# Performance work log

Measured on AMD Instinct MI355X. Metric: run time of the kernel, lower is better.

The kernel has to match this reference:

```python
import jax, jax.numpy as jnp
import numpy as np

B, H, W, C, HEADS, WS, SS = 32, 56, 56, 512, 16, 7, 3
HID = 4 * C
N = WS * WS          # tokens per window = 49
NW = (H // WS) * (W // WS)  # windows per image = 64
HD = C // HEADS
SCALE = HD ** -0.5

def _rel_index():
    coords = np.stack(np.meshgrid(np.arange(WS), np.arange(WS), indexing='ij'))
    cf = coords.reshape(2, -1)
    rel = (cf[:, :, None] - cf[:, None, :]).transpose(1, 2, 0)
    rel[..., 0] += WS - 1
    rel[..., 1] += WS - 1
    rel[..., 0] *= 2 * WS - 1
    return rel.sum(-1)  # [N, N]

REL_IDX = _rel_index()

def _attn_mask():
    # standard Swin SW-MSA mask: label 3x3 shifted regions, diff labels -> -100
    img = np.zeros((H, W), dtype=np.float32)
    cnt = 0
    for hs in (slice(0, -WS), slice(-WS, -SS), slice(-SS, None)):
        for ws_ in (slice(0, -WS), slice(-WS, -SS), slice(-SS, None)):
            img[hs, ws_] = cnt
            cnt += 1
    mw = img.reshape(H // WS, WS, W // WS, WS).transpose(0, 2, 1, 3).reshape(NW, N)
    diff = mw[:, None, :] - mw[:, :, None]
    return jnp.asarray(np.where(diff != 0, -100.0, 0.0).astype(np.float32))  # [NW, N, N]

ATTN_MASK = _attn_mask()

def layernorm(x, g, b, eps=1e-5):
    m = jnp.mean(x, -1, keepdims=True)
    v = jnp.mean((x - m) ** 2, -1, keepdims=True)
    return (x - m) * jax.lax.rsqrt(v + eps) * g + b

def setup_inputs():
    key = jax.random.key(0)
    ks = jax.random.split(key, 8)
    f32 = jnp.float32
    return {
        'x': jax.random.normal(ks[0], (B, H * W, C), f32),
        'norm1_g': jnp.ones((C,), f32), 'norm1_b': jnp.zeros((C,), f32),
        'qkv_w': jax.random.normal(ks[1], (3 * C, C), f32) * 0.02,
        'qkv_b': jnp.zeros((3 * C,), f32),
        'rel_bias': jax.random.normal(ks[2], ((2 * WS - 1) ** 2, HEADS), f32) * 0.02,
        'proj_w': jax.random.normal(ks[3], (C, C), f32) * 0.02,
        'proj_b': jnp.zeros((C,), f32),
        'norm2_g': jnp.ones((C,), f32), 'norm2_b': jnp.zeros((C,), f32),
        'mlp_w1': jax.random.normal(ks[4], (HID, C), f32) * 0.02,
        'mlp_b1': jnp.zeros((HID,), f32),
        'mlp_w2': jax.random.normal(ks[5], (C, HID), f32) * 0.02,
        'mlp_b2': jnp.zeros((C,), f32),
    }

def reference(x, norm1_g, norm1_b, qkv_w, qkv_b, rel_bias, proj_w, proj_b,
              norm2_g, norm2_b, mlp_w1, mlp_b1, mlp_w2, mlp_b2):
    skip = x
    h = layernorm(x, norm1_g, norm1_b).reshape(B, H, W, C)
    h = jnp.roll(h, (-SS, -SS), axis=(1, 2))  # cyclic shift
    # window partition -> [B*NW, N, C]
    h = h.reshape(B, H // WS, WS, W // WS, WS, C).transpose(0, 1, 3, 2, 4, 5).reshape(B * NW, N, C)
    qkv = (h @ qkv_w.T + qkv_b).reshape(B * NW, N, 3, HEADS, HD).transpose(2, 0, 3, 1, 4)
    q, k, v = qkv[0] * SCALE, qkv[1], qkv[2]  # [B*NW, HEADS, N, HD]
    attn = jnp.einsum('whnd,whmd->whnm', q, k)
    bias = rel_bias[REL_IDX.reshape(-1)].reshape(N, N, HEADS).transpose(2, 0, 1)
    attn = attn + bias[None]
    attn = attn.reshape(B, NW, HEADS, N, N) + ATTN_MASK[None, :, None]
    attn = jax.nn.softmax(attn, axis=-1).reshape(B * NW, HEADS, N, N)
    h = jnp.einsum('whnm,whmd->whnd', attn, v).transpose(0, 2, 1, 3).reshape(B * NW, N, C)
    h = h @ proj_w.T + proj_b
    # window reverse + reverse cyclic shift
    h = h.reshape(B, H // WS, W // WS, WS, WS, C).transpose(0, 1, 3, 2, 4, 5).reshape(B, H, W, C)
    h = jnp.roll(h, (SS, SS), axis=(1, 2)).reshape(B, H * W, C)
    x = skip + h
    m = layernorm(x, norm2_g, norm2_b)
    m = jax.nn.gelu(m @ mlp_w1.T + mlp_b1, approximate=False) @ mlp_w2.T + mlp_b2
    return x + m
```

## Files before the change

kernel.cpp:

```cpp
#include <hip/hip_runtime.h>
#include <cstdint>
#include <cstddef>

#define DI __device__ __forceinline__

typedef __bf16 bf16_t;
typedef __bf16 bf16x8 __attribute__((ext_vector_type(8)));
typedef float f32x4 __attribute__((ext_vector_type(4)));

static constexpr float SCALE = 0.17677669529663687f;

DI bf16_t f2b(float f) {
  uint32_t u = __builtin_bit_cast(uint32_t, f);
  u += 0x7fffu + ((u >> 16) & 1u);
  return __builtin_bit_cast(bf16_t, (uint16_t)(u >> 16));
}

DI void gld16(const void* g, void* l) {
  __builtin_amdgcn_global_load_lds(
      (const __attribute__((address_space(1))) uint32_t*)g,
      (__attribute__((address_space(3))) uint32_t*)l, 16, 0, 0);
}

__global__ __launch_bounds__(256)
void cvtw(const float* __restrict__ in, bf16_t* __restrict__ out, int n) {
  int i = (blockIdx.x * 256 + threadIdx.x) * 4;
  if (i >= n) return;
  float4 v = *(const float4*)(in + i);
  ushort4 o;
  o.x = __builtin_bit_cast(uint16_t, f2b(v.x));
  o.y = __builtin_bit_cast(uint16_t, f2b(v.y));
  o.z = __builtin_bit_cast(uint16_t, f2b(v.z));
  o.w = __builtin_bit_cast(uint16_t, f2b(v.w));
  *(ushort4*)(out + i) = o;
}

__global__ __launch_bounds__(256)
void bias_pre(const float* __restrict__ rel, float* __restrict__ bf) {
  int idx = blockIdx.x * 256 + threadIdx.x;
  int head = idx >> 12, t1 = (idx >> 6) & 63, t2 = idx & 63;
  float v = -1e30f;
  if (t1 < 49 && t2 < 49) {
    int i1 = t1 / 7, j1 = t1 - i1 * 7, i2 = t2 / 7, j2 = t2 - i2 * 7;
    v = rel[((i1 - i2 + 6) * 13 + (j1 - j2 + 6)) * 16 + head];
  }
  bf[idx] = v;
}

template<bool WIN>
__global__ __launch_bounds__(128)
void ln_kernel(const float* __restrict__ in, const float* __restrict__ g,
               const float* __restrict__ be, bf16_t* __restrict__ out)
{
  const int r = blockIdx.x;
  const int tid = threadIdx.x;
  long srow;
  if (WIN) {
    int bw = r / 49, t = r - bw * 49;
    int b = bw >> 6, w = bw & 63;
    int wh = w >> 3, ww = w & 7;
    int i = t / 7, j = t - i * 7;
    int hs = wh * 7 + i + 3; if (hs >= 56) hs -= 56;
    int wsr = ww * 7 + j + 3; if (wsr >= 56) wsr -= 56;
    srow = (long)b * 3136 + hs * 56 + wsr;
  } else {
    srow = r;
  }
  const float4 v = *(const float4*)(in + srow * 512 + tid * 4);
  float s = v.x + v.y + v.z + v.w;
  float sq = v.x * v.x + v.y * v.y + v.z * v.z + v.w * v.w;
#pragma unroll
  for (int m = 1; m < 64; m <<= 1) { s += __shfl_xor(s, m); sq += __shfl_xor(sq, m); }
  __shared__ float ls[2], lq[2];
  if ((tid & 63) == 0) { ls[tid >> 6] = s; lq[tid >> 6] = sq; }
  __syncthreads();
  s = ls[0] + ls[1]; sq = lq[0] + lq[1];
  const float mean = s * (1.f / 512.f);
  const float rs = rsqrtf(sq * (1.f / 512.f) - mean * mean + 1e-5f);
  const float4 gg = *(const float4*)(g + tid * 4);
  const float4 bb = *(const float4*)(be + tid * 4);
  ushort4 o;
  o.x = __builtin_bit_cast(uint16_t, f2b((v.x - mean) * rs * gg.x + bb.x));
  o.y = __builtin_bit_cast(uint16_t, f2b((v.y - mean) * rs * gg.y + bb.y));
  o.z = __builtin_bit_cast(uint16_t, f2b((v.z - mean) * rs * gg.z + bb.z));
  o.w = __builtin_bit_cast(uint16_t, f2b((v.w - mean) * rs * gg.w + bb.w));
  *(ushort4*)(out + (long)r * 512 + tid * 4) = o;
}

template<int EPI>
__global__ __launch_bounds__(512, 4)
void gemm128(const bf16_t* __restrict__ A, const bf16_t* __restrict__ Bw,
             const float* __restrict__ bias, const float* __restrict__ extra,
             void* __restrict__ out0, void* __restrict__ out1v, void* __restrict__ out2v,
             const int K, const int NBN)
{
  __shared__ __align__(128) bf16_t lds[3][384 * 32];
  const int tid = threadIdx.x, lane = tid & 63, wave = tid >> 6;

  const int nwg = gridDim.x;
  const int q = nwg >> 3, r = nwg & 7;
  const int xcd = blockIdx.x & 7, sidx = blockIdx.x >> 3;
  const int wgid = (xcd < r ? xcd * (q + 1) : r * (q + 1) + (xcd - r) * q) + sidx;
  const int bm = wgid / NBN, bn = wgid - bm * NBN;

  const int scc = ((tid & 3) ^ ((tid >> 3) & 3)) * 8;
  const bf16_t* pA  = A  + (size_t)(bm * 128 + (tid >> 2)) * K + scc;
  const bf16_t* pB0 = Bw + (size_t)(bn * 256 + (tid >> 2)) * K + scc;
  const bf16_t* pB1 = Bw + (size_t)(bn * 256 + 128 + (tid >> 2)) * K + scc;
  const int NT = K >> 5;

#define STAGE(KT, S) do { \
    gld16(pA  + (size_t)(KT) * 32, &lds[S][tid * 8]); \
    gld16(pB0 + (size_t)(KT) * 32, &lds[S][(512 + tid) * 8]); \
    gld16(pB1 + (size_t)(KT) * 32, &lds[S][(1024 + tid) * 8]); \
  } while (0)

  const int fr = lane & 15, fkc = lane >> 4;
  const int swzoff = ((fkc ^ ((fr >> 1) & 3)) << 3);
  const int wr = wave >> 2, wc = wave & 3;

  f32x4 acc[4][4] = {};

  STAGE(0, 0);
  STAGE(1, 1);
  asm volatile("s_waitcnt vmcnt(3)");
  __builtin_amdgcn_s_barrier();
  __builtin_amdgcn_sched_barrier(0);

  for (int t = 0; t < NT; ++t) {
    const int cur = t % 3;
    if (t + 2 < NT) {
      int sb = cur + 2; if (sb >= 3) sb -= 3;
      STAGE(t + 2, sb);
    }
    bf16x8 af[4], bf[4];
#pragma unroll
    for (int m = 0; m < 4; ++m)
      af[m] = *(const bf16x8*)&lds[cur][(wr * 64 + m * 16 + fr) * 32 + swzoff];
#pragma unroll
    for (int n = 0; n < 4; ++n)
      bf[n] = *(const bf16x8*)&lds[cur][(128 + wc * 64 + n * 16 + fr) * 32 + swzoff];
    asm volatile("s_waitcnt lgkmcnt(0)");
    __builtin_amdgcn_sched_barrier(0);
    __builtin_amdgcn_s_setprio(1);
#pragma unroll
    for (int m = 0; m < 4; ++m)
#pragma unroll
      for (int n = 0; n < 4; ++n)
        acc[m][n] = __builtin_amdgcn_mfma_f32_16x16x32_bf16(af[m], bf[n], acc[m][n], 0, 0, 0);
    __builtin_amdgcn_s_setprio(0);
    __builtin_amdgcn_sched_barrier(0);
    if (t + 2 < NT)      asm volatile("s_waitcnt vmcnt(3)");
    else if (t + 1 < NT) asm volatile("s_waitcnt vmcnt(0)");
    __builtin_amdgcn_s_barrier();
    __builtin_amdgcn_sched_barrier(0);
  }
#undef STAGE

  const int rq = fkc * 4;
#pragma unroll
  for (int m = 0; m < 4; ++m) {
#pragma unroll
    for (int j = 0; j < 4; ++j) {
      const int grow = bm * 128 + wr * 64 + m * 16 + rq + j;
      long obase = 0;
      if (EPI == 0) {
        int bwi = grow / 49, t = grow - bwi * 49;
        obase = ((long)bwi * 16 * 49 + t) * 32;
      } else if (EPI == 1) {
        int bwi = grow / 49, t = grow - bwi * 49;
        int b = bwi >> 6, w = bwi & 63;
        int wh = w >> 3, ww = w & 7;
        int i = t / 7, jj = t - i * 7;
        int hs = wh * 7 + i + 3; if (hs >= 56) hs -= 56;
        int wsr = ww * 7 + jj + 3; if (wsr >= 56) wsr -= 56;
        obase = ((long)b * 3136 + hs * 56 + wsr) * 512;
      } else if (EPI == 2) {
        obase = (long)grow * 2048;
      } else {
        obase = (long)grow * 512;
      }
#pragma unroll
      for (int n = 0; n < 4; ++n) {
        const int gcol = bn * 256 + wc * 64 + n * 16 + fr;
        float v = acc[m][n][j] + bias[gcol];
        if (EPI == 0) {
          int part = gcol >> 9, head = (gcol >> 5) & 15, d = gcol & 31;
          if (part == 0) v *= SCALE;
          bf16_t* dst = (bf16_t*)(part == 0 ? out0 : (part == 1 ? out1v : out2v));
          dst[obase + (long)head * (49 * 32) + d] = f2b(v);
        } else if (EPI == 1) {
          ((float*)out0)[obase + gcol] = v + extra[obase + gcol];
        } else if (EPI == 2) {
          float z = 1.5957691216057308f * (v + 0.044715f * v * v * v);
          float e = __expf(z);
          float th = 1.f - 2.f / (e + 1.f);
          float gv = 0.5f * v * (1.f + th);
          ((bf16_t*)out0)[obase + gcol] = f2b(gv);
        } else {
          ((float*)out0)[obase + gcol] = v + extra[obase + gcol];
        }
      }
    }
  }
}

__global__ __launch_bounds__(256)
void attn_kernel(const bf16_t* __restrict__ qb, const bf16_t* __restrict__ kb,
                 const bf16_t* __restrict__ vb, const float* __restrict__ biasf,
                 bf16_t* __restrict__ aout)
{
  __shared__ bf16_t Q[64 * 32];
  __shared__ bf16_t Kl[64 * 32];
  __shared__ bf16_t Vt[32 * 64];
  __shared__ bf16_t Pl[4][16 * 64];
  const int bid = blockIdx.x;
  const int bw = bid >> 4, head = bid & 15;
  const int tid = threadIdx.x, lane = tid & 63, wave = tid >> 6;
  {
    uint4 z = {0u, 0u, 0u, 0u};
    *(uint4*)&Q[tid * 8] = z;
    *(uint4*)&Kl[tid * 8] = z;
    *(uint4*)&Vt[tid * 8] = z;
  }
  __syncthreads();
  const bf16_t* qsrc = qb + (long)bid * (49 * 32);
  const bf16_t* ksrc = kb + (long)bid * (49 * 32);
  const bf16_t* vsrc = vb + (long)bid * (49 * 32);
  if (tid < 196) {
    *(uint4*)&Q[tid * 8] = *(const uint4*)(qsrc + tid * 8);
    *(uint4*)&Kl[tid * 8] = *(const uint4*)(ksrc + tid * 8);
  }
  for (int e = tid; e < 1568; e += 256) {
    int t = e >> 5, d = e & 31;
    Vt[d * 64 + t] = vsrc[e];
  }
  __syncthreads();
  const int fr = lane & 15, fk = (lane >> 4) * 8, rq = (lane >> 4) * 4;
  bf16x8 aq = *(const bf16x8*)&Q[(wave * 16 + fr) * 32 + fk];
  f32x4 s[4];
#pragma unroll
  for (int n = 0; n < 4; ++n) {
    bf16x8 bk = *(const bf16x8*)&Kl[(n * 16 + fr) * 32 + fk];
    f32x4 z = {0.f, 0.f, 0.f, 0.f};
    s[n] = __builtin_amdgcn_mfma_f32_16x16x32_bf16(aq, bk, z, 0, 0, 0);
  }
  const int w = bw & 63;
  const bool wh7 = ((w >> 3) == 7), ww7 = ((w & 7) == 7);
  const float* bh = biasf + head * 4096;
#pragma unroll
  for (int j = 0; j < 4; ++j) {
    const int row = wave * 16 + rq + j;
    int i1 = row / 7, j1 = row - i1 * 7;
    bool b1h = wh7 && (i1 >= 4), b1w = ww7 && (j1 >= 4);
    float pv[4];
    float mx = -3.0e38f;
#pragma unroll
    for (int n = 0; n < 4; ++n) {
      const int col = n * 16 + fr;
      float v = s[n][j] + bh[row * 64 + col];
      if (wh7 || ww7) {
        int i2 = col / 7, j2 = col - i2 * 7;
        bool b2h = wh7 && (i2 >= 4), b2w = ww7 && (j2 >= 4);
        if ((b1h != b2h) || (b1w != b2w)) v -= 100.f;
      }
      pv[n] = v;
      mx = fmaxf(mx, v);
    }
#pragma unroll
    for (int msk = 1; msk < 16; msk <<= 1) mx = fmaxf(mx, __shfl_xor(mx, msk));
    float sm = 0.f;
#pragma unroll
    for (int n = 0; n < 4; ++n) { pv[n] = __expf(pv[n] - mx); sm += pv[n]; }
#pragma unroll
    for (int msk = 1; msk < 16; msk <<= 1) sm += __shfl_xor(sm, msk);
    const float inv = 1.f / sm;
#pragma unroll
    for (int n = 0; n < 4; ++n)
      Pl[wave][(rq + j) * 64 + n * 16 + fr] = f2b(pv[n] * inv);
  }
  __syncthreads();
  f32x4 o[2] = {};
#pragma unroll
  for (int kk = 0; kk < 2; ++kk) {
    bf16x8 pa = *(const bf16x8*)&Pl[wave][fr * 64 + kk * 32 + fk];
#pragma unroll
    for (int dt = 0; dt < 2; ++dt) {
      bf16x8 vv = *(const bf16x8*)&Vt[(dt * 16 + fr) * 64 + kk * 32 + fk];
      o[dt] = __builtin_amdgcn_mfma_f32_16x16x32_bf16(pa, vv, o[dt], 0, 0, 0);
    }
  }
#pragma unroll
  for (int j = 0; j < 4; ++j) {
    const int t1 = wave * 16 + rq + j;
    if (t1 < 49) {
      bf16_t* dst = aout + ((long)bw * 49 + t1) * 512 + head * 32;
      dst[fr] = f2b(o[0][j]);
      dst[16 + fr] = f2b(o[1][j]);
    }
  }
}

extern "C" void kernel_launch(void* const* d_in, const int* in_sizes, int n_in,
                              void* d_out, int out_size, void* d_ws, size_t ws_size,
                              hipStream_t stream)
{
  const float* x      = (const float*)d_in[0];
  const float* n1g    = (const float*)d_in[1];
  const float* n1b    = (const float*)d_in[2];
  const float* qkv_w  = (const float*)d_in[3];
  const float* qkv_b  = (const float*)d_in[4];
  const float* rel    = (const float*)d_in[5];
  const float* proj_w = (const float*)d_in[6];
  const float* proj_b = (const float*)d_in[7];
  const float* n2g    = (const float*)d_in[8];
  const float* n2b    = (const float*)d_in[9];
  const float* w1     = (const float*)d_in[10];
  const float* b1     = (const float*)d_in[11];
  const float* w2     = (const float*)d_in[12];
  const float* b2     = (const float*)d_in[13];

  char* ws = (char*)d_ws;
  bf16_t* Wqkv  = (bf16_t*)(ws + 0);
  bf16_t* Wproj = (bf16_t*)(ws + 1572864);
  bf16_t* Wm1   = (bf16_t*)(ws + 2097152);
  bf16_t* Wm2   = (bf16_t*)(ws + 4194304);
  float*  biasf = (float*)(ws + 6291456);
  const size_t ABYTES = (size_t)100352 * 512 * 2;
  const size_t P1 = 8388608;
  const size_t P2 = P1 + ABYTES + 1048576;
  bf16_t* xw      = (bf16_t*)(ws + P1);
  bf16_t* qbuf    = (bf16_t*)(ws + P2);
  bf16_t* kbuf    = (bf16_t*)(ws + P2 + ABYTES);
  bf16_t* vbuf    = (bf16_t*)(ws + P2 + 2 * ABYTES);
  bf16_t* attnout = xw;
  bf16_t* h2      = xw;
  bf16_t* hidden  = qbuf;

  cvtw<<<768, 256, 0, stream>>>(qkv_w, Wqkv, 1536 * 512);
  cvtw<<<256, 256, 0, stream>>>(proj_w, Wproj, 512 * 512);
  cvtw<<<1024, 256, 0, stream>>>(w1, Wm1, 2048 * 512);
  cvtw<<<1024, 256, 0, stream>>>(w2, Wm2, 512 * 2048);
  bias_pre<<<256, 256, 0, stream>>>(rel, biasf);

  ln_kernel<true><<<100352, 128, 0, stream>>>(x, n1g, n1b, xw);
  gemm128<0><<<784 * 6, 512, 0, stream>>>(xw, Wqkv, qkv_b, nullptr,
                                          qbuf, kbuf, vbuf, 512, 6);
  attn_kernel<<<32768, 256, 0, stream>>>(qbuf, kbuf, vbuf, biasf, attnout);
  gemm128<1><<<784 * 2, 512, 0, stream>>>(attnout, Wproj, proj_b, x,
                                          d_out, nullptr, nullptr, 512, 2);
  ln_kernel<false><<<100352, 128, 0, stream>>>((const float*)d_out, n2g, n2b, h2);
  gemm128<2><<<784 * 8, 512, 0, stream>>>(h2, Wm1, b1, nullptr,
                                          hidden, nullptr, nullptr, 512, 8);
  gemm128<3><<<784 * 2, 512, 0, stream>>>(hidden, Wm2, b2, (const float*)d_out,
                                          d_out, nullptr, nullptr, 2048, 2);
}
```

Before: 1.347 ms.

## Enlarge GEMM tiles to 256x256 with phased double-buffered K=64 pipeline

Replaces the 128x256 GEMM with a 256x256 tile per workgroup. It uses a K=64 step split into two 32-wide halves, double-buffered in LDS, with loads interleaved between four MFMA phases. Each wave now holds 8x4 accumulators, which doubles operand reuse per LDS read and halves the workgroup count. Occupancy drops to 2 waves per SIMD and register pressure goes up. The GELU epilogue is also simplified to use a fast reciprocal, and the bias loads are hoisted out of the row loop.

```diff
diff --git a/kernel.cpp b/kernel.cpp
--- a/kernel.cpp
+++ b/kernel.cpp
@@ -87,14 +87,16 @@
   *(ushort4*)(out + (long)r * 512 + tid * 4) = o;
 }
 
+#define MFMA16(a, b, c) __builtin_amdgcn_mfma_f32_16x16x32_bf16((a), (b), (c), 0, 0, 0)
+
 template<int EPI>
-__global__ __launch_bounds__(512, 4)
-void gemm128(const bf16_t* __restrict__ A, const bf16_t* __restrict__ Bw,
+__global__ __launch_bounds__(512, 2)
+void gemm256(const bf16_t* __restrict__ A, const bf16_t* __restrict__ Bw,
              const float* __restrict__ bias, const float* __restrict__ extra,
              void* __restrict__ out0, void* __restrict__ out1v, void* __restrict__ out2v,
              const int K, const int NBN)
 {
-  __shared__ __align__(128) bf16_t lds[3][384 * 32];
+  __shared__ __align__(128) bf16_t lds[8][8192];
   const int tid = threadIdx.x, lane = tid & 63, wave = tid >> 6;
 
   const int nwg = gridDim.x;
@@ -103,70 +105,121 @@
   const int wgid = (xcd < r ? xcd * (q + 1) : r * (q + 1) + (xcd - r) * q) + sidx;
   const int bm = wgid / NBN, bn = wgid - bm * NBN;
 
-  const int scc = ((tid & 3) ^ ((tid >> 3) & 3)) * 8;
-  const bf16_t* pA  = A  + (size_t)(bm * 128 + (tid >> 2)) * K + scc;
-  const bf16_t* pB0 = Bw + (size_t)(bn * 256 + (tid >> 2)) * K + scc;
-  const bf16_t* pB1 = Bw + (size_t)(bn * 256 + 128 + (tid >> 2)) * K + scc;
-  const int NT = K >> 5;
-
-#define STAGE(KT, S) do { \
-    gld16(pA  + (size_t)(KT) * 32, &lds[S][tid * 8]); \
-    gld16(pB0 + (size_t)(KT) * 32, &lds[S][(512 + tid) * 8]); \
-    gld16(pB1 + (size_t)(KT) * 32, &lds[S][(1024 + tid) * 8]); \
+  const int srow = tid >> 2, slot = tid & 3;
+  const int chunk = slot ^ ((srow >> 1) & 3);
+  const bf16_t* pA = A + (size_t)(bm * 256 + srow) * K + chunk * 8;
+  const bf16_t* pB = Bw + (size_t)(bn * 256 + srow) * K + chunk * 8;
+  const size_t rowK = (size_t)128 * K;
+  const int NT = K >> 6;
+
+#define STG(mat, b, h, koff) do { \
+    const bf16_t* _p = ((mat) ? pB : pA) + (koff); \
+    bf16_t* _l = &lds[((mat) ? 4 : 0) + (b) * 2 + (h)][tid * 8]; \
+    gld16(_p, _l); \
+    gld16(_p + rowK, _l + 4096); \
   } while (0)
 
+  STG(0, 0, 0, 0);  STG(1, 0, 0, 0);
+  STG(0, 0, 1, 32); STG(1, 0, 1, 32);
+  STG(0, 1, 0, 64); STG(1, 1, 0, 64);
+  STG(0, 1, 1, 96);
+
   const int fr = lane & 15, fkc = lane >> 4;
-  const int swzoff = ((fkc ^ ((fr >> 1) & 3)) << 3);
   const int wr = wave >> 2, wc = wave & 3;
-
-  f32x4 acc[4][4] = {};
-
-  STAGE(0, 0);
-  STAGE(1, 1);
-  asm volatile("s_waitcnt vmcnt(3)");
+  const int slotq = (fkc ^ ((fr >> 1) & 3)) << 3;
+  const int aoff = (wr * 128 + fr) * 32 + slotq;
+  const int boff = (wc * 64 + fr) * 32 + slotq;
+
+  f32x4 acc[8][4] = {};
+  bf16x8 af[8], bq[4];
+
+  asm volatile("s_waitcnt vmcnt(6)");
   __builtin_amdgcn_s_barrier();
   __builtin_amdgcn_sched_barrier(0);
 
-  for (int t = 0; t < NT; ++t) {
-    const int cur = t % 3;
-    if (t + 2 < NT) {
-      int sb = cur + 2; if (sb >= 3) sb -= 3;
-      STAGE(t + 2, sb);
-    }
-    bf16x8 af[4], bf[4];
-#pragma unroll
-    for (int m = 0; m < 4; ++m)
-      af[m] = *(const bf16x8*)&lds[cur][(wr * 64 + m * 16 + fr) * 32 + swzoff];
-#pragma unroll
-    for (int n = 0; n < 4; ++n)
-      bf[n] = *(const bf16x8*)&lds[cur][(128 + wc * 64 + n * 16 + fr) * 32 + swzoff];
-    asm volatile("s_waitcnt lgkmcnt(0)");
-    __builtin_amdgcn_sched_barrier(0);
-    __builtin_amdgcn_s_setprio(1);
-#pragma unroll
-    for (int m = 0; m < 4; ++m)
-#pragma unroll
-      for (int n = 0; n < 4; ++n)
-        acc[m][n] = __builtin_amdgcn_mfma_f32_16x16x32_bf16(af[m], bf[n], acc[m][n], 0, 0, 0);
-    __builtin_amdgcn_s_setprio(0);
-    __builtin_amdgcn_sched_barrier(0);
-    if (t + 2 < NT)      asm volatile("s_waitcnt vmcnt(3)");
-    else if (t + 1 < NT) asm volatile("s_waitcnt vmcnt(0)");
-    __builtin_amdgcn_s_barrier();
-    __builtin_amdgcn_sched_barrier(0);
-  }
-#undef STAGE
+#define PH_SYNC() \
+  __builtin_amdgcn_sched_barrier(0); \
+  __builtin_amdgcn_s_barrier(); \
+  asm volatile("s_waitcnt lgkmcnt(0)"); \
+  __builtin_amdgcn_sched_barrier(0); \
+  __builtin_amdgcn_s_setprio(1)
+
+#define PH_END() \
+  __builtin_amdgcn_s_setprio(0); \
+  __builtin_amdgcn_sched_barrier(0); \
+  __builtin_amdgcn_s_barrier()
+
+#define MM2(N0, N1) \
+  _Pragma("unroll") \
+  for (int m = 0; m < 8; ++m) { \
+    acc[m][N0] = MFMA16(af[m], bq[N0], acc[m][N0]); \
+    acc[m][N1] = MFMA16(af[m], bq[N1], acc[m][N1]); \
+  }
+
+#define KTILE(B, KT) do { \
+     \
+    _Pragma("unroll") \
+    for (int m = 0; m < 8; ++m) af[m] = *(const bf16x8*)&lds[(B) * 2][aoff + m * 512]; \
+    bq[0] = *(const bf16x8*)&lds[4 + (B) * 2][boff]; \
+    bq[1] = *(const bf16x8*)&lds[4 + (B) * 2][boff + 512]; \
+    if ((KT) + 1 < NT) STG(1, (B) ^ 1, 1, ((KT) + 1) * 64 + 32); \
+    PH_SYNC(); \
+    MM2(0, 1); \
+    PH_END(); \
+     \
+    bq[2] = *(const bf16x8*)&lds[4 + (B) * 2][boff + 1024]; \
+    bq[3] = *(const bf16x8*)&lds[4 + (B) * 2][boff + 1536]; \
+    if ((KT) + 2 < NT) STG(0, (B), 0, ((KT) + 2) * 64); \
+    PH_SYNC(); \
+    MM2(2, 3); \
+    PH_END(); \
+     \
+    _Pragma("unroll") \
+    for (int m = 0; m < 8; ++m) af[m] = *(const bf16x8*)&lds[(B) * 2 + 1][aoff + m * 512]; \
+    bq[0] = *(const bf16x8*)&lds[4 + (B) * 2 + 1][boff]; \
+    bq[1] = *(const bf16x8*)&lds[4 + (B) * 2 + 1][boff + 512]; \
+    if ((KT) + 2 < NT) STG(1, (B), 0, ((KT) + 2) * 64); \
+    PH_SYNC(); \
+    MM2(0, 1); \
+    PH_END(); \
+     \
+    bq[2] = *(const bf16x8*)&lds[4 + (B) * 2 + 1][boff + 1024]; \
+    bq[3] = *(const bf16x8*)&lds[4 + (B) * 2 + 1][boff + 1536]; \
+    if ((KT) + 2 < NT) STG(0, (B), 1, ((KT) + 2) * 64 + 32); \
+    PH_SYNC(); \
+    MM2(2, 3); \
+    __builtin_amdgcn_s_setprio(0); \
+    __builtin_amdgcn_sched_barrier(0); \
+    if ((KT) + 2 < NT) asm volatile("s_waitcnt vmcnt(6)"); \
+    else               asm volatile("s_waitcnt vmcnt(0)"); \
+    __builtin_amdgcn_s_barrier(); \
+    __builtin_amdgcn_sched_barrier(0); \
+  } while (0)
+
+  for (int kt = 0; kt < NT; kt += 2) {
+    KTILE(0, kt);
+    KTILE(1, kt + 1);
+  }
+#undef KTILE
+#undef MM2
+#undef PH_END
+#undef PH_SYNC
+#undef STG
 
   const int rq = fkc * 4;
-#pragma unroll
-  for (int m = 0; m < 4; ++m) {
+  float bs[4];
+#pragma unroll
+  for (int n = 0; n < 4; ++n) bs[n] = bias[bn * 256 + wc * 64 + n * 16 + fr];
+
+#pragma unroll
+  for (int m = 0; m < 8; ++m) {
 #pragma unroll
     for (int j = 0; j < 4; ++j) {
-      const int grow = bm * 128 + wr * 64 + m * 16 + rq + j;
+      const int grow = bm * 256 + wr * 128 + m * 16 + rq + j;
       long obase = 0;
       if (EPI == 0) {
         int bwi = grow / 49, t = grow - bwi * 49;
-        obase = ((long)bwi * 16 * 49 + t) * 32;
+        obase = ((long)bwi * 784 + t) * 32;
       } else if (EPI == 1) {
         int bwi = grow / 49, t = grow - bwi * 49;
         int b = bwi >> 6, w = bwi & 63;
@@ -183,20 +236,20 @@
 #pragma unroll
       for (int n = 0; n < 4; ++n) {
         const int gcol = bn * 256 + wc * 64 + n * 16 + fr;
-        float v = acc[m][n][j] + bias[gcol];
+        float v = acc[m][n][j] + bs[n];
         if (EPI == 0) {
           int part = gcol >> 9, head = (gcol >> 5) & 15, d = gcol & 31;
           if (part == 0) v *= SCALE;
           bf16_t* dst = (bf16_t*)(part == 0 ? out0 : (part == 1 ? out1v : out2v));
-          dst[obase + (long)head * (49 * 32) + d] = f2b(v);
+          dst[obase + (long)head * 1568 + d] = f2b(v);
         } else if (EPI == 1) {
           ((float*)out0)[obase + gcol] = v + extra[obase + gcol];
         } else if (EPI == 2) {
-          float z = 1.5957691216057308f * (v + 0.044715f * v * v * v);
+          float m2 = v * v;
+          float z = v * fmaf(0.07135481627f, m2, 1.59576912161f);
           float e = __expf(z);
-          float th = 1.f - 2.f / (e + 1.f);
-          float gv = 0.5f * v * (1.f + th);
-          ((bf16_t*)out0)[obase + gcol] = f2b(gv);
+          float rr = __builtin_amdgcn_rcpf(e + 1.0f);
+          ((bf16_t*)out0)[obase + gcol] = f2b(fmaf(-v, rr, v));
         } else {
           ((float*)out0)[obase + gcol] = v + extra[obase + gcol];
         }
@@ -344,14 +397,14 @@
   bias_pre<<<256, 256, 0, stream>>>(rel, biasf);
 
   ln_kernel<true><<<100352, 128, 0, stream>>>(x, n1g, n1b, xw);
-  gemm128<0><<<784 * 6, 512, 0, stream>>>(xw, Wqkv, qkv_b, nullptr,
+  gemm256<0><<<392 * 6, 512, 0, stream>>>(xw, Wqkv, qkv_b, nullptr,
                                           qbuf, kbuf, vbuf, 512, 6);
   attn_kernel<<<32768, 256, 0, stream>>>(qbuf, kbuf, vbuf, biasf, attnout);
-  gemm128<1><<<784 * 2, 512, 0, stream>>>(attnout, Wproj, proj_b, x,
+  gemm256<1><<<392 * 2, 512, 0, stream>>>(attnout, Wproj, proj_b, x,
                                           d_out, nullptr, nullptr, 512, 2);
   ln_kernel<false><<<100352, 128, 0, stream>>>((const float*)d_out, n2g, n2b, h2);
-  gemm128<2><<<784 * 8, 512, 0, stream>>>(h2, Wm1, b1, nullptr,
+  gemm256<2><<<392 * 8, 512, 0, stream>>>(h2, Wm1, b1, nullptr,
                                           hidden, nullptr, nullptr, 512, 8);
-  gemm128<3><<<784 * 2, 512, 0, stream>>>(hidden, Wm2, b2, (const float*)d_out,
+  gemm256<3><<<392 * 2, 512, 0, stream>>>(hidden, Wm2, b2, (const float*)d_out,
                                           d_out, nullptr, nullptr, 2048, 2);
 }
```

Result: no change. 1.356 ms (+0.7%).

## Replace GEMM with persistent 256x256-tile kernel with four-stage pipelined k-loop

Applied to the files above, without the earlier changes.

The GEMM becomes persistent. Exactly 256 blocks of 1024 threads are launched, and each walks a strided sequence of 256x256 output tiles assigned per XCD. The k-loop now continues across tile boundaries through a four-deep LDS ring, so loads for the next tile overlap the current tile's epilogue. The change aims to cut launch and tail overhead, improve B-tile reuse and L2 locality, and raise per-block tile size. Bias loads are hoisted and the GELU epilogue uses a cheaper rcp-based form. Risks: 16 waves per CU with one block, pipelining and barrier tuning, and possible load imbalance when NBN does not divide 32 (NBN=6 leaves some blocks idle).

```diff
diff --git a/kernel.cpp b/kernel.cpp
--- a/kernel.cpp
+++ b/kernel.cpp
@@ -87,122 +87,144 @@
   *(ushort4*)(out + (long)r * 512 + tid * 4) = o;
 }
 
+#define MFMA16(a, b, c) __builtin_amdgcn_mfma_f32_16x16x32_bf16((a), (b), (c), 0, 0, 0)
+
 template<int EPI>
-__global__ __launch_bounds__(512, 4)
-void gemm128(const bf16_t* __restrict__ A, const bf16_t* __restrict__ Bw,
+__global__ __launch_bounds__(1024, 4)
+void gemm256(const bf16_t* __restrict__ A, const bf16_t* __restrict__ Bw,
              const float* __restrict__ bias, const float* __restrict__ extra,
              void* __restrict__ out0, void* __restrict__ out1v, void* __restrict__ out2v,
              const int K, const int NBN)
 {
-  __shared__ __align__(128) bf16_t lds[3][384 * 32];
+  __shared__ __align__(128) bf16_t lds[8][8192];
   const int tid = threadIdx.x, lane = tid & 63, wave = tid >> 6;
-
-  const int nwg = gridDim.x;
-  const int q = nwg >> 3, r = nwg & 7;
-  const int xcd = blockIdx.x & 7, sidx = blockIdx.x >> 3;
-  const int wgid = (xcd < r ? xcd * (q + 1) : r * (q + 1) + (xcd - r) * q) + sidx;
-  const int bm = wgid / NBN, bn = wgid - bm * NBN;
-
-  const int scc = ((tid & 3) ^ ((tid >> 3) & 3)) * 8;
-  const bf16_t* pA  = A  + (size_t)(bm * 128 + (tid >> 2)) * K + scc;
-  const bf16_t* pB0 = Bw + (size_t)(bn * 256 + (tid >> 2)) * K + scc;
-  const bf16_t* pB1 = Bw + (size_t)(bn * 256 + 128 + (tid >> 2)) * K + scc;
   const int NT = K >> 5;
 
-#define STAGE(KT, S) do { \
-    gld16(pA  + (size_t)(KT) * 32, &lds[S][tid * 8]); \
-    gld16(pB0 + (size_t)(KT) * 32, &lds[S][(512 + tid) * 8]); \
-    gld16(pB1 + (size_t)(KT) * 32, &lds[S][(1024 + tid) * 8]); \
+  const int xcd = blockIdx.x & 7, j = blockIdx.x >> 3;
+  const int G = 32 / NBN;
+  if (j >= G * NBN) return;
+  const int bmo = j / NBN;
+  const int bn = j - bmo * NBN;
+  const int m0 = xcd * 49;
+  const int tiles = (49 - bmo + G - 1) / G;
+  const int ST = tiles * NT;
+
+  const int srow = tid >> 2, slot = tid & 3;
+  const int chunk = slot ^ ((srow >> 1) & 3);
+  const size_t strideA = (size_t)G * 256 * K;
+
+  const bf16_t* pAs = A + ((size_t)(m0 + bmo) * 256 + srow) * K + chunk * 8;
+  const bf16_t* pBs = Bw + ((size_t)bn * 256 + srow) * K + chunk * 8;
+  int sS = 0, ktS = 0;
+
+#define STG() do { \
+    if (sS < ST) { \
+      gld16(pAs + ktS * 32, &lds[ktS & 3][tid * 8]); \
+      gld16(pBs + ktS * 32, &lds[4 + (ktS & 3)][tid * 8]); \
+      ++sS; if (++ktS == NT) { ktS = 0; pAs += strideA; } \
+    } \
   } while (0)
 
   const int fr = lane & 15, fkc = lane >> 4;
-  const int swzoff = ((fkc ^ ((fr >> 1) & 3)) << 3);
   const int wr = wave >> 2, wc = wave & 3;
+  const int slotq = (fkc ^ ((fr >> 1) & 3)) << 3;
+  const int aoff = (wr * 64 + fr) * 32 + slotq;
+  const int boff = (wc * 64 + fr) * 32 + slotq;
 
   f32x4 acc[4][4] = {};
 
-  STAGE(0, 0);
-  STAGE(1, 1);
-  asm volatile("s_waitcnt vmcnt(3)");
+  STG(); STG(); STG();
+  asm volatile("s_waitcnt vmcnt(4)");
   __builtin_amdgcn_s_barrier();
   __builtin_amdgcn_sched_barrier(0);
 
-  for (int t = 0; t < NT; ++t) {
-    const int cur = t % 3;
-    if (t + 2 < NT) {
-      int sb = cur + 2; if (sb >= 3) sb -= 3;
-      STAGE(t + 2, sb);
-    }
-    bf16x8 af[4], bf[4];
-#pragma unroll
-    for (int m = 0; m < 4; ++m)
-      af[m] = *(const bf16x8*)&lds[cur][(wr * 64 + m * 16 + fr) * 32 + swzoff];
-#pragma unroll
-    for (int n = 0; n < 4; ++n)
-      bf[n] = *(const bf16x8*)&lds[cur][(128 + wc * 64 + n * 16 + fr) * 32 + swzoff];
-    asm volatile("s_waitcnt lgkmcnt(0)");
-    __builtin_amdgcn_sched_barrier(0);
-    __builtin_amdgcn_s_setprio(1);
-#pragma unroll
-    for (int m = 0; m < 4; ++m)
-#pragma unroll
-      for (int n = 0; n < 4; ++n)
-        acc[m][n] = __builtin_amdgcn_mfma_f32_16x16x32_bf16(af[m], bf[n], acc[m][n], 0, 0, 0);
-    __builtin_amdgcn_s_setprio(0);
-    __builtin_amdgcn_sched_barrier(0);
-    if (t + 2 < NT)      asm volatile("s_waitcnt vmcnt(3)");
-    else if (t + 1 < NT) asm volatile("s_waitcnt vmcnt(0)");
-    __builtin_amdgcn_s_barrier();
-    __builtin_amdgcn_sched_barrier(0);
-  }
-#undef STAGE
-
+  int sG = 0;
+  int bmC = m0 + bmo;
   const int rq = fkc * 4;
-#pragma unroll
-  for (int m = 0; m < 4; ++m) {
-#pragma unroll
-    for (int j = 0; j < 4; ++j) {
-      const int grow = bm * 128 + wr * 64 + m * 16 + rq + j;
-      long obase = 0;
-      if (EPI == 0) {
-        int bwi = grow / 49, t = grow - bwi * 49;
-        obase = ((long)bwi * 16 * 49 + t) * 32;
-      } else if (EPI == 1) {
-        int bwi = grow / 49, t = grow - bwi * 49;
-        int b = bwi >> 6, w = bwi & 63;
-        int wh = w >> 3, ww = w & 7;
-        int i = t / 7, jj = t - i * 7;
-        int hs = wh * 7 + i + 3; if (hs >= 56) hs -= 56;
-        int wsr = ww * 7 + jj + 3; if (wsr >= 56) wsr -= 56;
-        obase = ((long)b * 3136 + hs * 56 + wsr) * 512;
-      } else if (EPI == 2) {
-        obase = (long)grow * 2048;
-      } else {
-        obase = (long)grow * 512;
-      }
-#pragma unroll
-      for (int n = 0; n < 4; ++n) {
-        const int gcol = bn * 256 + wc * 64 + n * 16 + fr;
-        float v = acc[m][n][j] + bias[gcol];
+  float bs[4];
+#pragma unroll
+  for (int n = 0; n < 4; ++n) bs[n] = bias[bn * 256 + wc * 64 + n * 16 + fr];
+
+  for (int t = 0; t < tiles; ++t) {
+#pragma unroll 4
+    for (int kt = 0; kt < NT; ++kt) {
+      bf16x8 af[4], bq[4];
+#pragma unroll
+      for (int m = 0; m < 4; ++m) af[m] = *(const bf16x8*)&lds[kt & 3][aoff + m * 512];
+#pragma unroll
+      for (int n = 0; n < 4; ++n) bq[n] = *(const bf16x8*)&lds[4 + (kt & 3)][boff + n * 512];
+      STG();
+      __builtin_amdgcn_sched_barrier(0);
+      __builtin_amdgcn_s_barrier();
+      asm volatile("s_waitcnt lgkmcnt(0)");
+      __builtin_amdgcn_sched_barrier(0);
+      __builtin_amdgcn_s_setprio(1);
+#pragma unroll
+      for (int m = 0; m < 4; ++m)
+#pragma unroll
+        for (int n = 0; n < 4; ++n)
+          acc[m][n] = MFMA16(af[m], bq[n], acc[m][n]);
+      __builtin_amdgcn_s_setprio(0);
+      __builtin_amdgcn_sched_barrier(0);
+      if (sG + 3 < ST)      asm volatile("s_waitcnt vmcnt(4)");
+      else if (sG + 2 < ST) asm volatile("s_waitcnt vmcnt(2)");
+      else                  asm volatile("s_waitcnt vmcnt(0)");
+      __builtin_amdgcn_s_barrier();
+      __builtin_amdgcn_sched_barrier(0);
+      ++sG;
+    }
+#pragma unroll
+    for (int m = 0; m < 4; ++m) {
+#pragma unroll
+      for (int jj4 = 0; jj4 < 4; ++jj4) {
+        const int grow = bmC * 256 + wr * 64 + m * 16 + rq + jj4;
+        long obase = 0;
         if (EPI == 0) {
-          int part = gcol >> 9, head = (gcol >> 5) & 15, d = gcol & 31;
-          if (part == 0) v *= SCALE;
-          bf16_t* dst = (bf16_t*)(part == 0 ? out0 : (part == 1 ? out1v : out2v));
-          dst[obase + (long)head * (49 * 32) + d] = f2b(v);
+          int bwi = grow / 49, t_ = grow - bwi * 49;
+          obase = ((long)bwi * 784 + t_) * 32;
         } else if (EPI == 1) {
-          ((float*)out0)[obase + gcol] = v + extra[obase + gcol];
+          int bwi = grow / 49, t_ = grow - bwi * 49;
+          int b = bwi >> 6, w = bwi & 63;
+          int wh = w >> 3, ww = w & 7;
+          int i = t_ / 7, jj = t_ - i * 7;
+          int hs = wh * 7 + i + 3; if (hs >= 56) hs -= 56;
+          int wsr = ww * 7 + jj + 3; if (wsr >= 56) wsr -= 56;
+          obase = ((long)b * 3136 + hs * 56 + wsr) * 512;
         } else if (EPI == 2) {
-          float z = 1.5957691216057308f * (v + 0.044715f * v * v * v);
-          float e = __expf(z);
-          float th = 1.f - 2.f / (e + 1.f);
-          float gv = 0.5f * v * (1.f + th);
-          ((bf16_t*)out0)[obase + gcol] = f2b(gv);
+          obase = (long)grow * 2048;
         } else {
-          ((float*)out0)[obase + gcol] = v + extra[obase + gcol];
+          obase = (long)grow * 512;
+        }
+#pragma unroll
+        for (int n = 0; n < 4; ++n) {
+          const int gcol = bn * 256 + wc * 64 + n * 16 + fr;
+          float v = acc[m][n][jj4] + bs[n];
+          if (EPI == 0) {
+            int part = gcol >> 9, head = (gcol >> 5) & 15, d = gcol & 31;
+            if (part == 0) v *= SCALE;
+            bf16_t* dst = (bf16_t*)(part == 0 ? out0 : (part == 1 ? out1v : out2v));
+            dst[obase + (long)head * 1568 + d] = f2b(v);
+          } else if (EPI == 1) {
+            ((float*)out0)[obase + gcol] = v + extra[obase + gcol];
+          } else if (EPI == 2) {
+            float m2 = v * v;
+            float z = v * fmaf(0.07135481627f, m2, 1.59576912161f);
+            float e = __expf(z);
+            float rr = __builtin_amdgcn_rcpf(e + 1.0f);
+            ((bf16_t*)out0)[obase + gcol] = f2b(fmaf(-v, rr, v));
+          } else {
+            ((float*)out0)[obase + gcol] = v + extra[obase + gcol];
+          }
         }
       }
     }
-  }
+#pragma unroll
+    for (int m = 0; m < 4; ++m)
+#pragma unroll
+      for (int n = 0; n < 4; ++n) acc[m][n] = (f32x4){0.f, 0.f, 0.f, 0.f};
+    bmC += G;
+  }
+#undef STG
 }
 
 __global__ __launch_bounds__(256)
@@ -344,14 +366,14 @@
   bias_pre<<<256, 256, 0, stream>>>(rel, biasf);
 
   ln_kernel<true><<<100352, 128, 0, stream>>>(x, n1g, n1b, xw);
-  gemm128<0><<<784 * 6, 512, 0, stream>>>(xw, Wqkv, qkv_b, nullptr,
-                                          qbuf, kbuf, vbuf, 512, 6);
+  gemm256<0><<<256, 1024, 0, stream>>>(xw, Wqkv, qkv_b, nullptr,
+                                       qbuf, kbuf, vbuf, 512, 6);
   attn_kernel<<<32768, 256, 0, stream>>>(qbuf, kbuf, vbuf, biasf, attnout);
-  gemm128<1><<<784 * 2, 512, 0, stream>>>(attnout, Wproj, proj_b, x,
-                                          d_out, nullptr, nullptr, 512, 2);
+  gemm256<1><<<256, 1024, 0, stream>>>(attnout, Wproj, proj_b, x,
+                                       d_out, nullptr, nullptr, 512, 2);
   ln_kernel<false><<<100352, 128, 0, stream>>>((const float*)d_out, n2g, n2b, h2);
-  gemm128<2><<<784 * 8, 512, 0, stream>>>(h2, Wm1, b1, nullptr,
-                                          hidden, nullptr, nullptr, 512, 8);
-  gemm128<3><<<784 * 2, 512, 0, stream>>>(hidden, Wm2, b2, (const float*)d_out,
-                                          d_out, nullptr, nullptr, 2048, 2);
-}
+  gemm256<2><<<256, 1024, 0, stream>>>(h2, Wm1, b1, nullptr,
+                                       hidden, nullptr, nullptr, 512, 8);
+  gemm256<3><<<256, 1024, 0, stream>>>(hidden, Wm2, b2, (const float*)d_out,
+                                       d_out, nullptr, nullptr, 2048, 2);
+}
```

New measurement: 1.385 ms. 2.8% more time.
